# Kernel optimization log

Measured on AMD Instinct MI355X. Metric: run time of the kernel, lower is better.

Reference implementation:

```python
import jax, jax.numpy as jnp
import numpy as np
from jax import lax

B, C, H, W = 16, 256, 96, 96
G, K, RED = 4, 3, 4


def setup_inputs() -> dict:
    key = jax.random.key(0)
    ks = jax.random.split(key, 8)
    return {
        "x": jax.random.normal(ks[0], (B, C, H, W), jnp.float32),
        "w_k": jax.random.normal(ks[1], (G, C, K, K), jnp.float32) * 0.02,
        "b_k": jax.random.normal(ks[2], (G, C), jnp.float32) * 0.02,
        "w1": jax.random.normal(ks[3], (C // RED, C), jnp.float32) * 0.05,
        "b1": jax.random.normal(ks[4], (C // RED,), jnp.float32) * 0.02,
        "bn_g": jnp.ones((C // RED,), jnp.float32),
        "bn_b": jnp.zeros((C // RED,), jnp.float32),
        "bn_m": jnp.zeros((C // RED,), jnp.float32),
        "bn_v": jnp.ones((C // RED,), jnp.float32),
        "w2": jax.random.normal(ks[5], (C * G, C // RED), jnp.float32) * 0.05,
        "b2": jax.random.normal(ks[6], (C * G,), jnp.float32) * 0.02,
    }


def reference(x, w_k, b_k, w1, b1, bn_g, bn_b, bn_m, bn_v, w2, b2):
    eps = 1e-5

    def proj(t):  # t: (B, C, h, w) -> (B, C*G, h, w)
        h = jnp.einsum('oc,bchw->bohw', w1, t) + b1[None, :, None, None]
        h = (h - bn_m[None, :, None, None]) * (bn_g / jnp.sqrt(bn_v + eps))[None, :, None, None] + bn_b[None, :, None, None]
        h = jax.nn.gelu(h, approximate=False)
        return jnp.einsum('oc,bchw->bohw', w2, h) + b2[None, :, None, None]

    # AdaptiveAvgPool2d((K, K)) with H, W divisible by K -> uniform block mean
    pooled = x.reshape(B, C, K, H // K, K, W // K).mean(axis=(3, 5))  # (B, C, K, K)
    scale = proj(pooled).reshape(B, G, C, K, K)
    scale = jax.nn.softmax(scale, axis=1)
    weight = jnp.einsum('bgckl,gckl->bckl', scale, w_k)  # (B, C, K, K) dynamic depthwise kernels

    # dynamic bias from global average pooling
    s2 = proj(x.mean(axis=(2, 3), keepdims=True)).reshape(B, G, C)
    s2 = jax.nn.softmax(s2, axis=1)
    bias = jnp.einsum('bgc,gc->bc', s2, b_k)  # (B, C)

    pad = K // 2

    def conv_one(xb, wb):  # xb (C,H,W), wb (C,K,K): depthwise conv, SAME padding
        return lax.conv_general_dilated(
            xb[None], wb[:, None], window_strides=(1, 1),
            padding=[(pad, pad), (pad, pad)], feature_group_count=C)[0]

    out = jax.vmap(conv_one)(x, weight) + bias[:, :, None, None]
    return out
```

## Files before the change

kernel.cpp:

```cpp
#include <hip/hip_runtime.h>
#include <math.h>

#define BB 16
#define CC 256
#define HH 96
#define WW 96
#define GG 4
#define KK 3
#define CR 64

__global__ __launch_bounds__(256) void pool_kernel(const float* __restrict__ x,
                                                   float* __restrict__ pooled) {
    const int bc = blockIdx.x;
    const float4* p4 = (const float4*)(x + (size_t)bc * (HH * WW));
    const int tid  = threadIdx.x;
    const int lane = tid & 63;
    const int wv   = tid >> 6;
    __shared__ float red[4];

    const int r_in = tid >> 3;
    const int c4   = tid & 7;

    #pragma unroll
    for (int bi = 0; bi < 3; ++bi) {
        #pragma unroll
        for (int bj = 0; bj < 3; ++bj) {
            const int row = bi * 32 + r_in;
            const int idx = row * 24 + bj * 8 + c4;
            float4 v = p4[idx];
            float s = v.x + v.y + v.z + v.w;
            #pragma unroll
            for (int off = 32; off > 0; off >>= 1) s += __shfl_down(s, off, 64);
            if (lane == 0) red[wv] = s;
            __syncthreads();
            if (tid == 0)
                pooled[bc * 9 + bi * 3 + bj] =
                    (red[0] + red[1] + red[2] + red[3]) * (1.0f / 1024.0f);
            __syncthreads();
        }
    }
}

__global__ __launch_bounds__(256) void proj_kernel(
    const float* __restrict__ pooled,
    const float* __restrict__ w1, const float* __restrict__ b1,
    const float* __restrict__ bn_g, const float* __restrict__ bn_b,
    const float* __restrict__ bn_m, const float* __restrict__ bn_v,
    const float* __restrict__ w2, const float* __restrict__ b2,
    const float* __restrict__ w_k, const float* __restrict__ b_k,
    float* __restrict__ weight, float* __restrict__ bias) {
    const int b = blockIdx.x / 10;
    const int p = blockIdx.x % 10;
    const int tid = threadIdx.x;

    __shared__ float t[CC];
    __shared__ float hbuf[CR];
    __shared__ float hpart[256];

    if (p < 9) {
        t[tid] = pooled[(b * CC + tid) * 9 + p];
    } else {
        float s = 0.f;
        #pragma unroll
        for (int q = 0; q < 9; ++q) s += pooled[(b * CC + tid) * 9 + q];
        t[tid] = s * (1.0f / 9.0f);
    }
    __syncthreads();

    const int o = tid & 63, part = tid >> 6;
    {
        const float* w1row = w1 + o * CC + part * 64;
        const float* tp = t + part * 64;
        float acc = 0.f;
        #pragma unroll
        for (int k = 0; k < 64; ++k) acc += w1row[k] * tp[k];
        hpart[tid] = acc;
    }
    __syncthreads();
    if (tid < 64) {
        float hsum = hpart[tid] + hpart[tid + 64] + hpart[tid + 128] +
                     hpart[tid + 192] + b1[tid];
        float hn = (hsum - bn_m[tid]) * (bn_g[tid] * rsqrtf(bn_v[tid] + 1e-5f)) + bn_b[tid];
        hbuf[tid] = 0.5f * hn * (1.0f + erff(hn * 0.70710678118654752f));
    }
    __syncthreads();

    float vals[4];
    #pragma unroll
    for (int q = 0; q < 4; ++q) {
        const int j = q * 256 + tid;
        const float* w2row = w2 + j * 64;
        float a = b2[j];
        #pragma unroll
        for (int o2 = 0; o2 < 64; ++o2) a += w2row[o2] * hbuf[o2];
        vals[q] = a;
    }
    float m = fmaxf(fmaxf(vals[0], vals[1]), fmaxf(vals[2], vals[3]));
    float e[4], sum = 0.f;
    #pragma unroll
    for (int q = 0; q < 4; ++q) { e[q] = expf(vals[q] - m); sum += e[q]; }
    const float rinv = 1.0f / sum;

    if (p < 9) {
        float ws = 0.f;
        #pragma unroll
        for (int q = 0; q < 4; ++q)
            ws += (e[q] * rinv) * w_k[(q * CC + tid) * 9 + p];
        weight[(b * CC + tid) * 9 + p] = ws;
    } else {
        float bs = 0.f;
        #pragma unroll
        for (int q = 0; q < 4; ++q)
            bs += (e[q] * rinv) * b_k[q * CC + tid];
        bias[b * CC + tid] = bs;
    }
}

__global__ __launch_bounds__(256) void dwconv_kernel(
    const float* __restrict__ x, const float* __restrict__ weight,
    const float* __restrict__ bias, float* __restrict__ out) {
    const int bc = blockIdx.x;
    const float* plane = x + (size_t)bc * (HH * WW);
    float* oplane = out + (size_t)bc * (HH * WW);
    __shared__ __align__(16) float tile[HH * WW];
    const int tid = threadIdx.x;

    {
        const float4* p4 = (const float4*)plane;
        float4* t4 = (float4*)tile;
        #pragma unroll
        for (int i = 0; i < 9; ++i) t4[tid + 256 * i] = p4[tid + 256 * i];
    }
    float wgt[9];
    #pragma unroll
    for (int k = 0; k < 9; ++k) wgt[k] = weight[bc * 9 + k];
    const float bs = bias[bc];
    __syncthreads();

    #pragma unroll 4
    for (int i = 0; i < 36; ++i) {
        const int p = tid + 256 * i;
        const int h = p / 96;
        const int w = p - h * 96;
        float acc = bs;
        #pragma unroll
        for (int dh = -1; dh <= 1; ++dh) {
            const int hh = h + dh;
            const bool hok = (unsigned)hh < 96u;
            #pragma unroll
            for (int dw = -1; dw <= 1; ++dw) {
                const int ww = w + dw;
                const bool ok = hok && ((unsigned)ww < 96u);
                float v = ok ? tile[hh * 96 + ww] : 0.0f;
                acc += wgt[(dh + 1) * 3 + (dw + 1)] * v;
            }
        }
        oplane[p] = acc;
    }
}

extern "C" void kernel_launch(void* const* d_in, const int* in_sizes, int n_in,
                              void* d_out, int out_size, void* d_ws, size_t ws_size,
                              hipStream_t stream) {
    const float* x    = (const float*)d_in[0];
    const float* w_k  = (const float*)d_in[1];
    const float* b_k  = (const float*)d_in[2];
    const float* w1   = (const float*)d_in[3];
    const float* b1   = (const float*)d_in[4];
    const float* bn_g = (const float*)d_in[5];
    const float* bn_b = (const float*)d_in[6];
    const float* bn_m = (const float*)d_in[7];
    const float* bn_v = (const float*)d_in[8];
    const float* w2   = (const float*)d_in[9];
    const float* b2   = (const float*)d_in[10];
    float* out = (float*)d_out;

    float* pooled = (float*)d_ws;
    float* weight = pooled + BB * CC * 9;
    float* bias   = weight + BB * CC * 9;

    pool_kernel<<<BB * CC, 256, 0, stream>>>(x, pooled);
    proj_kernel<<<BB * 10, 256, 0, stream>>>(pooled, w1, b1, bn_g, bn_b, bn_m,
                                             bn_v, w2, b2, w_k, b_k, weight, bias);
    dwconv_kernel<<<BB * CC, 256, 0, stream>>>(x, weight, bias, out);
}
```

Before: 329.7 us.

## Use padded halo tile with float4 stencil outputs in dwconv and batch pool reductions

The depthwise conv now loads each plane into a zero-padded shared tile (stride 104), so boundary checks go away. Each thread computes four adjacent outputs, reading one float4 plus two scalars per row and writing a float4 store. The pool kernel does all nine loads first and reduces with a single barrier instead of eighteen. The projection dot products use float4 loads. The padded tile uses slightly more LDS, and the unaligned scalar halo reads may cause bank conflicts.

```diff
diff --git a/kernel.cpp b/kernel.cpp
--- a/kernel.cpp
+++ b/kernel.cpp
@@ -5,9 +5,7 @@
 #define CC 256
 #define HH 96
 #define WW 96
-#define GG 4
-#define KK 3
-#define CR 64
+#define TS 104
 
 __global__ __launch_bounds__(256) void pool_kernel(const float* __restrict__ x,
                                                    float* __restrict__ pooled) {
@@ -16,29 +14,30 @@
     const int tid  = threadIdx.x;
     const int lane = tid & 63;
     const int wv   = tid >> 6;
-    __shared__ float red[4];
-
     const int r_in = tid >> 3;
     const int c4   = tid & 7;
-
-    #pragma unroll
-    for (int bi = 0; bi < 3; ++bi) {
+    __shared__ float red[9][4];
+
+    float s[9];
+    #pragma unroll
+    for (int bi = 0; bi < 3; ++bi)
         #pragma unroll
         for (int bj = 0; bj < 3; ++bj) {
-            const int row = bi * 32 + r_in;
-            const int idx = row * 24 + bj * 8 + c4;
-            float4 v = p4[idx];
-            float s = v.x + v.y + v.z + v.w;
-            #pragma unroll
-            for (int off = 32; off > 0; off >>= 1) s += __shfl_down(s, off, 64);
-            if (lane == 0) red[wv] = s;
-            __syncthreads();
-            if (tid == 0)
-                pooled[bc * 9 + bi * 3 + bj] =
-                    (red[0] + red[1] + red[2] + red[3]) * (1.0f / 1024.0f);
-            __syncthreads();
-        }
-    }
+            float4 v = p4[(bi * 32 + r_in) * 24 + bj * 8 + c4];
+            s[bi * 3 + bj] = v.x + v.y + v.z + v.w;
+        }
+
+    #pragma unroll
+    for (int k = 0; k < 9; ++k) {
+        float t = s[k];
+        #pragma unroll
+        for (int off = 32; off; off >>= 1) t += __shfl_down(t, off, 64);
+        if (lane == 0) red[k][wv] = t;
+    }
+    __syncthreads();
+    if (tid < 9)
+        pooled[bc * 9 + tid] =
+            (red[tid][0] + red[tid][1] + red[tid][2] + red[tid][3]) * (1.0f / 1024.0f);
 }
 
 __global__ __launch_bounds__(256) void proj_kernel(
@@ -53,8 +52,8 @@
     const int p = blockIdx.x % 10;
     const int tid = threadIdx.x;
 
-    __shared__ float t[CC];
-    __shared__ float hbuf[CR];
+    __shared__ __align__(16) float t[CC];
+    __shared__ __align__(16) float hbuf[64];
     __shared__ float hpart[256];
 
     if (p < 9) {
@@ -69,11 +68,14 @@
 
     const int o = tid & 63, part = tid >> 6;
     {
-        const float* w1row = w1 + o * CC + part * 64;
-        const float* tp = t + part * 64;
+        const float4* w1r = (const float4*)(w1 + o * CC + part * 64);
+        const float4* tp  = (const float4*)(t + part * 64);
         float acc = 0.f;
         #pragma unroll
-        for (int k = 0; k < 64; ++k) acc += w1row[k] * tp[k];
+        for (int k = 0; k < 16; ++k) {
+            float4 a = w1r[k], v = tp[k];
+            acc += a.x * v.x + a.y * v.y + a.z * v.z + a.w * v.w;
+        }
         hpart[tid] = acc;
     }
     __syncthreads();
@@ -89,10 +91,14 @@
     #pragma unroll
     for (int q = 0; q < 4; ++q) {
         const int j = q * 256 + tid;
-        const float* w2row = w2 + j * 64;
+        const float4* w2r = (const float4*)(w2 + j * 64);
+        const float4* hb  = (const float4*)hbuf;
         float a = b2[j];
         #pragma unroll
-        for (int o2 = 0; o2 < 64; ++o2) a += w2row[o2] * hbuf[o2];
+        for (int k = 0; k < 16; ++k) {
+            float4 wv = w2r[k], hv = hb[k];
+            a += wv.x * hv.x + wv.y * hv.y + wv.z * hv.z + wv.w * hv.w;
+        }
         vals[q] = a;
     }
     float m = fmaxf(fmaxf(vals[0], vals[1]), fmaxf(vals[2], vals[3]));
@@ -122,40 +128,54 @@
     const int bc = blockIdx.x;
     const float* plane = x + (size_t)bc * (HH * WW);
     float* oplane = out + (size_t)bc * (HH * WW);
-    __shared__ __align__(16) float tile[HH * WW];
+    __shared__ __align__(16) float tile[98 * TS];
     const int tid = threadIdx.x;
+
+    if (tid < 98) {
+        tile[tid * TS + 3]   = 0.f;
+        tile[tid * TS + 100] = 0.f;
+        tile[3 + tid]            = 0.f;
+        tile[97 * TS + 3 + tid]  = 0.f;
+    }
+
+    float wgt[9];
+    #pragma unroll
+    for (int k = 0; k < 9; ++k) wgt[k] = weight[bc * 9 + k];
+    const float bs = bias[bc];
 
     {
         const float4* p4 = (const float4*)plane;
         float4* t4 = (float4*)tile;
         #pragma unroll
-        for (int i = 0; i < 9; ++i) t4[tid + 256 * i] = p4[tid + 256 * i];
-    }
-    float wgt[9];
-    #pragma unroll
-    for (int k = 0; k < 9; ++k) wgt[k] = weight[bc * 9 + k];
-    const float bs = bias[bc];
-    __syncthreads();
-
-    #pragma unroll 4
-    for (int i = 0; i < 36; ++i) {
-        const int p = tid + 256 * i;
-        const int h = p / 96;
-        const int w = p - h * 96;
-        float acc = bs;
-        #pragma unroll
-        for (int dh = -1; dh <= 1; ++dh) {
-            const int hh = h + dh;
-            const bool hok = (unsigned)hh < 96u;
-            #pragma unroll
-            for (int dw = -1; dw <= 1; ++dw) {
-                const int ww = w + dw;
-                const bool ok = hok && ((unsigned)ww < 96u);
-                float v = ok ? tile[hh * 96 + ww] : 0.0f;
-                acc += wgt[(dh + 1) * 3 + (dw + 1)] * v;
-            }
-        }
-        oplane[p] = acc;
+        for (int i = 0; i < 9; ++i) {
+            const int idx4 = tid + 256 * i;
+            const int r = idx4 / 24;
+            const int c4 = idx4 - r * 24;
+            t4[(r + 1) * (TS / 4) + 1 + c4] = p4[idx4];
+        }
+    }
+    __syncthreads();
+
+    #pragma unroll
+    for (int j = 0; j < 9; ++j) {
+        const int s = tid + 256 * j;
+        const int h = s / 24;
+        const int wq = s - h * 24;
+        const int cb = 4 + 4 * wq;
+        float4 acc = {bs, bs, bs, bs};
+        #pragma unroll
+        for (int r = 0; r < 3; ++r) {
+            const int a = (h + r) * TS + cb;
+            const float4 m = *(const float4*)(tile + a);
+            const float L = tile[a - 1];
+            const float R = tile[a + 4];
+            const float wl = wgt[r * 3 + 0], wc = wgt[r * 3 + 1], wr = wgt[r * 3 + 2];
+            acc.x += wl * L   + wc * m.x + wr * m.y;
+            acc.y += wl * m.x + wc * m.y + wr * m.z;
+            acc.z += wl * m.y + wc * m.z + wr * m.w;
+            acc.w += wl * m.z + wc * m.w + wr * R;
+        }
+        *(float4*)(oplane + 4 * s) = acc;
     }
 }
 
```

New measurement: 317.2 us. 1.04x faster.
